# Kernel tuning notes

Measured on AMD Instinct MI355X. Metric: run time of the kernel, lower is better.

## Reference

```python
import jax, jax.numpy as jnp
import numpy as np

T, B, IN_DIM, D_VALUE, D_KEY = 1024, 8, 512, 64, 64
EPS = 1e-8

def setup_inputs() -> dict:
    key = jax.random.key(0)
    ks = jax.random.split(key, 7)
    s = 1.0 / np.sqrt(IN_DIM)
    return {
        "x":  jax.random.normal(ks[0], (T, B, IN_DIM), dtype=jnp.float32),
        "Wv": jax.random.uniform(ks[1], (D_VALUE, IN_DIM), jnp.float32, -s, s),
        "bv": jax.random.uniform(ks[2], (D_VALUE,), jnp.float32, -s, s),
        "Wk": jax.random.uniform(ks[3], (D_KEY, IN_DIM), jnp.float32, -s, s),
        "bk": jax.random.uniform(ks[4], (D_KEY,), jnp.float32, -s, s),
        "Wa": jax.random.uniform(ks[5], (D_KEY, IN_DIM), jnp.float32, -s, s),
        "ba": jax.random.uniform(ks[6], (D_KEY,), jnp.float32, -s, s),
    }

def reference(x, Wv, bv, Wk, bk, Wa, ba):
    # Projections: x (T,B,in_dim) -> v (T,B,d), k (T,B,n), alpha (T,B,n)
    v = jnp.einsum('tbi,di->tbd', x, Wv) + bv
    k = jnp.einsum('tbi,ni->tbn', x, Wk) + bk
    alpha = jax.nn.sigmoid(jnp.einsum('tbi,ni->tbn', x, Wa) + ba)
    # outer product per timestep: (T,B,d,n)
    outer = jnp.einsum('tbd,tbn->tbdn', v, k)
    # log-space cumulative decay, normalized by final cumprod
    log_cumprod = jnp.cumsum(jnp.log(jnp.maximum(alpha, EPS)), axis=0)  # (T,B,n)
    cumprod = jnp.exp(log_cumprod)
    decay = cumprod / (cumprod[-1:] + EPS)
    weighted = outer * decay[:, :, None, :]  # (T,B,d,n)
    S = jnp.cumsum(weighted, axis=0)
    return S
```

## Files before the change

### kernel.cpp

```cpp
#include <hip/hip_runtime.h>
#include <math.h>

#define T_DIM  1024
#define B_DIM  8
#define IN_D   512
#define NROWS  (T_DIM * B_DIM)
#define EPSF   1e-8f
#define LOG_EPS (-18.4206807f)

#define CHUNK  16
#define NCHUNK (T_DIM / CHUNK)
#define SEG    16
#define NSEG   (T_DIM / SEG)

typedef float vfloat4 __attribute__((ext_vector_type(4)));

#define OFF_WT   0
#define OFF_V    (OFF_WT + IN_D * 192)
#define OFF_K    (OFF_V  + NROWS * 64)
#define OFF_Z    (OFF_K  + NROWS * 64)
#define OFF_SEG  (OFF_Z  + NROWS * 64)
#define OFF_TOT  (OFF_SEG + NSEG * B_DIM * 64)
#define OFF_P    (OFF_TOT + B_DIM * 64)
#define OFF_WB   (OFF_P + NCHUNK * B_DIM * 4096)

#define FMA4(A, W, C) \
    (C).x = fmaf((A), (W).x, (C).x); (C).y = fmaf((A), (W).y, (C).y); \
    (C).z = fmaf((A), (W).z, (C).z); (C).w = fmaf((A), (W).w, (C).w);

__global__ void k0_wt(const float* __restrict__ Wv, const float* __restrict__ Wk,
                      const float* __restrict__ Wa, float* __restrict__ Wt,
                      float* __restrict__ seg) {
    int idx = blockIdx.x * 256 + threadIdx.x;
    if (idx < NSEG * 512) seg[idx] = 0.f;
    int i = idx / 192, c = idx % 192;
    float v;
    if (c < 64)       v = Wv[c * IN_D + i];
    else if (c < 128) v = Wk[(c - 64) * IN_D + i];
    else              v = Wa[(c - 128) * IN_D + i];
    Wt[i * 192 + c] = v;
}

__global__ __launch_bounds__(256) void k1_proj(
        const float* __restrict__ x, const float* __restrict__ Wt,
        const float* __restrict__ bv, const float* __restrict__ bk, const float* __restrict__ ba,
        float* __restrict__ V, float* __restrict__ Kb, float* __restrict__ Zb,
        float* __restrict__ seg) {
    __shared__ float smem[14336];
    const int tid = threadIdx.x;
    const int h   = tid >> 6;
    const int sl  = h >> 1;
    const int kk0 = (h & 1) * 16;
    const int t6  = tid & 63;
    const int rq  = t6 >> 4;
    const int cq  = t6 & 15;
    const int row0 = blockIdx.x * 32;

    float4 acc[8][3];
#pragma unroll
    for (int j = 0; j < 8; ++j)
#pragma unroll
        for (int m = 0; m < 3; ++m) acc[j][m] = make_float4(0.f, 0.f, 0.f, 0.f);

    for (int s = 0; s < 8; ++s) {
#pragma unroll
        for (int q = 0; q < 2; ++q) {
            int idx = tid + q * 256;
            int hh = idx >> 8, r = idx & 31, f = (idx >> 5) & 7;
            float4 v4 = reinterpret_cast<const float4*>(x)[((row0 + r) * IN_D + hh * 256 + s * 32 + f * 4) >> 2];
            smem[hh * 1024 + (f * 4 + 0) * 32 + r] = v4.x;
            smem[hh * 1024 + (f * 4 + 1) * 32 + r] = v4.y;
            smem[hh * 1024 + (f * 4 + 2) * 32 + r] = v4.z;
            smem[hh * 1024 + (f * 4 + 3) * 32 + r] = v4.w;
        }
#pragma unroll
        for (int q = 0; q < 12; ++q) {
            int idx = tid + q * 256;
            int hh = idx / 1536;
            int rem = idx - hh * 1536;
            int kk = rem / 48;
            int f  = rem - kk * 48;
            float4 v4 = reinterpret_cast<const float4*>(Wt)[((hh * 256 + s * 32 + kk) * 192 + f * 4) >> 2];
            *reinterpret_cast<float4*>(&smem[2048 + hh * 6144 + kk * 192 + f * 4]) = v4;
        }
        __syncthreads();

#pragma unroll 4
        for (int k16 = 0; k16 < 16; ++k16) {
            const int kk = kk0 + k16;
            const float* xp = &smem[sl * 1024 + kk * 32 + rq * 8];
            float4 xv0 = *reinterpret_cast<const float4*>(xp);
            float4 xv1 = *reinterpret_cast<const float4*>(xp + 4);
            const float* wp = &smem[2048 + sl * 6144 + kk * 192 + cq * 4];
            float4 w0 = *reinterpret_cast<const float4*>(wp);
            float4 w1 = *reinterpret_cast<const float4*>(wp + 64);
            float4 w2 = *reinterpret_cast<const float4*>(wp + 128);
#pragma unroll
            for (int j = 0; j < 4; ++j) {
                float a0 = (&xv0.x)[j];
                float a1 = (&xv1.x)[j];
                FMA4(a0, w0, acc[j][0]); FMA4(a0, w1, acc[j][1]); FMA4(a0, w2, acc[j][2]);
                FMA4(a1, w0, acc[j + 4][0]); FMA4(a1, w1, acc[j + 4][1]); FMA4(a1, w2, acc[j + 4][2]);
            }
        }
        __syncthreads();
    }

    float* red = smem;
    if (h == 1 || h == 3) {
        float* rg = red + (h >> 1) * 6144;
#pragma unroll
        for (int jr = 0; jr < 8; ++jr)
#pragma unroll
            for (int m = 0; m < 3; ++m)
#pragma unroll
                for (int c = 0; c < 4; ++c)
                    rg[((jr * 3 + m) * 4 + c) * 64 + t6] = (&acc[jr][m].x)[c];
    }
    __syncthreads();
    if (h == 0 || h == 2) {
        float* rg = red + (h >> 1) * 6144;
#pragma unroll
        for (int jr = 0; jr < 8; ++jr)
#pragma unroll
            for (int m = 0; m < 3; ++m)
#pragma unroll
                for (int c = 0; c < 4; ++c)
                    (&acc[jr][m].x)[c] += rg[((jr * 3 + m) * 4 + c) * 64 + t6];
    }
    __syncthreads();
    if (h == 2) {
#pragma unroll
        for (int jr = 0; jr < 8; ++jr)
#pragma unroll
            for (int m = 0; m < 3; ++m)
#pragma unroll
                for (int c = 0; c < 4; ++c)
                    red[((jr * 3 + m) * 4 + c) * 64 + t6] = (&acc[jr][m].x)[c];
    }
    __syncthreads();
    if (h == 0) {
#pragma unroll
        for (int jr = 0; jr < 8; ++jr)
#pragma unroll
            for (int m = 0; m < 3; ++m)
#pragma unroll
                for (int c = 0; c < 4; ++c)
                    (&acc[jr][m].x)[c] += red[((jr * 3 + m) * 4 + c) * 64 + t6];

        float4 bv4 = *reinterpret_cast<const float4*>(&bv[cq * 4]);
        float4 bk4 = *reinterpret_cast<const float4*>(&bk[cq * 4]);
        float4 ba4 = *reinterpret_cast<const float4*>(&ba[cq * 4]);
#pragma unroll
        for (int jr = 0; jr < 8; ++jr) {
            int row = row0 + rq * 8 + jr;
            float4 r0, r1, z2, l4;
            r0.x = acc[jr][0].x + bv4.x; r0.y = acc[jr][0].y + bv4.y;
            r0.z = acc[jr][0].z + bv4.z; r0.w = acc[jr][0].w + bv4.w;
            r1.x = acc[jr][1].x + bk4.x; r1.y = acc[jr][1].y + bk4.y;
            r1.z = acc[jr][1].z + bk4.z; r1.w = acc[jr][1].w + bk4.w;
            z2.x = acc[jr][2].x + ba4.x; z2.y = acc[jr][2].y + ba4.y;
            z2.z = acc[jr][2].z + ba4.z; z2.w = acc[jr][2].w + ba4.w;
            l4.x = fmaxf(-log1pf(expf(-z2.x)), LOG_EPS);
            l4.y = fmaxf(-log1pf(expf(-z2.y)), LOG_EPS);
            l4.z = fmaxf(-log1pf(expf(-z2.z)), LOG_EPS);
            l4.w = fmaxf(-log1pf(expf(-z2.w)), LOG_EPS);
            *reinterpret_cast<float4*>(&V [row * 64 + cq * 4]) = r0;
            *reinterpret_cast<float4*>(&Kb[row * 64 + cq * 4]) = r1;
            *reinterpret_cast<float4*>(&Zb[row * 64 + cq * 4]) = l4;
            float* sp = &seg[(row >> 7) * 512 + (row & 7) * 64 + cq * 4];
            atomicAdd(sp + 0, l4.x);
            atomicAdd(sp + 1, l4.y);
            atomicAdd(sp + 2, l4.z);
            atomicAdd(sp + 3, l4.w);
        }
    }
}

__global__ __launch_bounds__(256) void k3_partial(const float* __restrict__ V,
                                                  const float* __restrict__ Z,
                                                  const float* __restrict__ seg,
                                                  const float* __restrict__ Kb,
                                                  float* __restrict__ P,
                                                  float* __restrict__ Wb) {
    __shared__ float vs[CHUNK * 64];
    __shared__ float wsh[CHUNK * 64];
    __shared__ float gsum[4 * 64];
    int b = blockIdx.x & 7, cch = blockIdx.x >> 3;
    int tid = threadIdx.x;
    int dg = tid >> 4, n4 = tid & 15;
    int n = tid & 63, g = tid >> 6;
    int base = b * 64 + n;
    int il = tid >> 4, f = tid & 15;

    float4 v4 = reinterpret_cast<const float4*>(V)[((cch * CHUNK + il) * 8 + b) * 16 + f];

    float run = 0.f, total = 0.f;
#pragma unroll 8
    for (int s2 = 0; s2 < NSEG; ++s2) {
        float sv = seg[s2 * 512 + base];
        if (s2 < cch) run += sv;
        total += sv;
    }
    float invden = 1.f / (expf(total) + EPSF);

    int t0 = cch * CHUNK + g * 4;
    float l0 = Z[(t0 + 0) * 512 + base];
    float l1 = Z[(t0 + 1) * 512 + base];
    float l2 = Z[(t0 + 2) * 512 + base];
    float l3 = Z[(t0 + 3) * 512 + base];
    float k0v = Kb[(t0 + 0) * 512 + base];
    float k1v = Kb[(t0 + 1) * 512 + base];
    float k2v = Kb[(t0 + 2) * 512 + base];
    float k3v = Kb[(t0 + 3) * 512 + base];
    gsum[g * 64 + n] = l0 + l1 + l2 + l3;
    reinterpret_cast<float4*>(vs)[il * 16 + f] = v4;
    __syncthreads();
    float pre = run;
#pragma unroll
    for (int g2 = 0; g2 < 3; ++g2) if (g2 < g) pre += gsum[g2 * 64 + n];
    float c0 = pre + l0, c1 = c0 + l1, c2 = c1 + l2, c3 = c2 + l3;
    wsh[(g * 4 + 0) * 64 + n] = k0v * expf(c0) * invden;
    wsh[(g * 4 + 1) * 64 + n] = k1v * expf(c1) * invden;
    wsh[(g * 4 + 2) * 64 + n] = k2v * expf(c2) * invden;
    wsh[(g * 4 + 3) * 64 + n] = k3v * expf(c3) * invden;
    __syncthreads();

    reinterpret_cast<float4*>(Wb)[(cch * 8 + b) * 256 + il * 16 + f] =
        reinterpret_cast<const float4*>(wsh)[il * 16 + f];

    float4 acc[4];
#pragma unroll
    for (int q = 0; q < 4; ++q) acc[q] = make_float4(0.f, 0.f, 0.f, 0.f);

#pragma unroll
    for (int i = 0; i < CHUNK; ++i) {
        float4 wv = reinterpret_cast<const float4*>(wsh)[i * 16 + n4];
#pragma unroll
        for (int q = 0; q < 4; ++q) {
            float vd = vs[i * 64 + dg + 16 * q];
            acc[q].x = fmaf(vd, wv.x, acc[q].x);
            acc[q].y = fmaf(vd, wv.y, acc[q].y);
            acc[q].z = fmaf(vd, wv.z, acc[q].z);
            acc[q].w = fmaf(vd, wv.w, acc[q].w);
        }
    }
    float* Pp = P + (cch * 8 + b) * 4096;
#pragma unroll
    for (int q = 0; q < 4; ++q)
        *reinterpret_cast<float4*>(Pp + (dg + 16 * q) * 64 + 4 * n4) = acc[q];
}

__global__ __launch_bounds__(256) void k4_prefix(float* __restrict__ P) {
    int gid = blockIdx.x * 256 + threadIdx.x;
    int b = gid >> 12, dn = gid & 4095;
    float run = 0.f;
#pragma unroll
    for (int c = 0; c < NCHUNK; ++c) {
        float v = P[(c * 8 + b) * 4096 + dn];
        P[(c * 8 + b) * 4096 + dn] = run;
        run += v;
    }
}

__global__ __launch_bounds__(256) void k5_main(const float* __restrict__ V,
                                               const float* __restrict__ Wb,
                                               const float* __restrict__ P,
                                               float* __restrict__ S) {
    __shared__ float vs[CHUNK * 64];
    __shared__ float wsh[CHUNK * 64];
    int b = blockIdx.x & 7, cch = blockIdx.x >> 3;
    int tid = threadIdx.x;
    int dg = tid >> 4, n4 = tid & 15;
    int il = tid >> 4, f = tid & 15;

    float4 v4 = reinterpret_cast<const float4*>(V)[((cch * CHUNK + il) * 8 + b) * 16 + f];
    float4 w4 = reinterpret_cast<const float4*>(Wb)[(cch * 8 + b) * 256 + il * 16 + f];
    vfloat4 acc[4];
    const float* Pp = P + (cch * 8 + b) * 4096;
#pragma unroll
    for (int q = 0; q < 4; ++q)
        acc[q] = *reinterpret_cast<const vfloat4*>(Pp + (dg + 16 * q) * 64 + 4 * n4);
    reinterpret_cast<float4*>(vs)[il * 16 + f]  = v4;
    reinterpret_cast<float4*>(wsh)[il * 16 + f] = w4;
    __syncthreads();

#pragma unroll
    for (int i = 0; i < CHUNK; ++i) {
        float4 wv = reinterpret_cast<const float4*>(wsh)[i * 16 + n4];
        int t = cch * CHUNK + i;
        float* Sb = S + (size_t)t * 32768 + b * 4096;
#pragma unroll
        for (int q = 0; q < 4; ++q) {
            float vd = vs[i * 64 + dg + 16 * q];
            acc[q].x = fmaf(vd, wv.x, acc[q].x);
            acc[q].y = fmaf(vd, wv.y, acc[q].y);
            acc[q].z = fmaf(vd, wv.z, acc[q].z);
            acc[q].w = fmaf(vd, wv.w, acc[q].w);
            __builtin_nontemporal_store(acc[q],
                reinterpret_cast<vfloat4*>(Sb + (dg + 16 * q) * 64 + 4 * n4));
        }
    }
}

extern "C" void kernel_launch(void* const* d_in, const int* in_sizes, int n_in,
                              void* d_out, int out_size, void* d_ws, size_t ws_size,
                              hipStream_t stream) {
    const float* x  = (const float*)d_in[0];
    const float* Wv = (const float*)d_in[1];
    const float* bv = (const float*)d_in[2];
    const float* Wk = (const float*)d_in[3];
    const float* bk = (const float*)d_in[4];
    const float* Wa = (const float*)d_in[5];
    const float* ba = (const float*)d_in[6];
    float* S  = (float*)d_out;
    float* ws = (float*)d_ws;

    float* Wt  = ws + OFF_WT;
    float* V   = ws + OFF_V;
    float* Kb  = ws + OFF_K;
    float* Zb  = ws + OFF_Z;
    float* seg = ws + OFF_SEG;
    float* P   = ws + OFF_P;
    float* Wb  = ws + OFF_WB;

    k0_wt     <<<384, 256, 0, stream>>>(Wv, Wk, Wa, Wt, seg);
    k1_proj   <<<256, 256, 0, stream>>>(x, Wt, bv, bk, ba, V, Kb, Zb, seg);
    k3_partial<<<512, 256, 0, stream>>>(V, Zb, seg, Kb, P, Wb);
    k4_prefix <<<128, 256, 0, stream>>>(P);
    k5_main   <<<512, 256, 0, stream>>>(V, Wb, P, S);
}
```

Baseline: 219.6 us.

## Fuse projection, partial, prefix and main kernels into one persistent kernel with grid barriers

```diff
diff --git a/kernel.cpp b/kernel.cpp
--- a/kernel.cpp
+++ b/kernel.cpp
@@ -12,6 +12,8 @@
 #define NCHUNK (T_DIM / CHUNK)
 #define SEG    16
 #define NSEG   (T_DIM / SEG)
+
+#define NBLK   512u
 
 typedef float vfloat4 __attribute__((ext_vector_type(4)));
 
@@ -23,16 +25,31 @@
 #define OFF_TOT  (OFF_SEG + NSEG * B_DIM * 64)
 #define OFF_P    (OFF_TOT + B_DIM * 64)
 #define OFF_WB   (OFF_P + NCHUNK * B_DIM * 4096)
+#define OFF_BAR  (OFF_WB + 524288)
 
 #define FMA4(A, W, C) \
     (C).x = fmaf((A), (W).x, (C).x); (C).y = fmaf((A), (W).y, (C).y); \
     (C).z = fmaf((A), (W).z, (C).z); (C).w = fmaf((A), (W).w, (C).w);
 
-__global__ void k0_wt(const float* __restrict__ Wv, const float* __restrict__ Wk,
-                      const float* __restrict__ Wa, float* __restrict__ Wt,
-                      float* __restrict__ seg) {
+__device__ __forceinline__ void gridbar(unsigned* bar, int slot) {
+    __threadfence();
+    __syncthreads();
+    if (threadIdx.x == 0) {
+        atomicAdd(&bar[slot], 1u);
+        while (__hip_atomic_load(&bar[slot], __ATOMIC_RELAXED,
+                                 __HIP_MEMORY_SCOPE_AGENT) < NBLK)
+            __builtin_amdgcn_s_sleep(2);
+        __threadfence();
+    }
+    __syncthreads();
+}
+
+__global__ void kpre(const float* __restrict__ Wv, const float* __restrict__ Wk,
+                     const float* __restrict__ Wa, float* __restrict__ Wt,
+                     float* __restrict__ seg, unsigned* __restrict__ bar) {
     int idx = blockIdx.x * 256 + threadIdx.x;
     if (idx < NSEG * 512) seg[idx] = 0.f;
+    if (idx < 16) bar[idx] = 0u;
     int i = idx / 192, c = idx % 192;
     float v;
     if (c < 64)       v = Wv[c * IN_D + i];
@@ -41,264 +58,266 @@
     Wt[i * 192 + c] = v;
 }
 
-__global__ __launch_bounds__(256) void k1_proj(
+__global__ __launch_bounds__(256, 2) void kfused(
         const float* __restrict__ x, const float* __restrict__ Wt,
         const float* __restrict__ bv, const float* __restrict__ bk, const float* __restrict__ ba,
         float* __restrict__ V, float* __restrict__ Kb, float* __restrict__ Zb,
-        float* __restrict__ seg) {
+        float* __restrict__ seg, float* __restrict__ P, float* __restrict__ Wb,
+        float* __restrict__ S, unsigned* __restrict__ bar) {
     __shared__ float smem[14336];
+    const int blk = blockIdx.x;
     const int tid = threadIdx.x;
-    const int h   = tid >> 6;
-    const int sl  = h >> 1;
-    const int kk0 = (h & 1) * 16;
-    const int t6  = tid & 63;
-    const int rq  = t6 >> 4;
-    const int cq  = t6 & 15;
-    const int row0 = blockIdx.x * 32;
-
-    float4 acc[8][3];
-#pragma unroll
-    for (int j = 0; j < 8; ++j)
-#pragma unroll
-        for (int m = 0; m < 3; ++m) acc[j][m] = make_float4(0.f, 0.f, 0.f, 0.f);
-
-    for (int s = 0; s < 8; ++s) {
-#pragma unroll
-        for (int q = 0; q < 2; ++q) {
-            int idx = tid + q * 256;
-            int hh = idx >> 8, r = idx & 31, f = (idx >> 5) & 7;
-            float4 v4 = reinterpret_cast<const float4*>(x)[((row0 + r) * IN_D + hh * 256 + s * 32 + f * 4) >> 2];
-            smem[hh * 1024 + (f * 4 + 0) * 32 + r] = v4.x;
-            smem[hh * 1024 + (f * 4 + 1) * 32 + r] = v4.y;
-            smem[hh * 1024 + (f * 4 + 2) * 32 + r] = v4.z;
-            smem[hh * 1024 + (f * 4 + 3) * 32 + r] = v4.w;
-        }
-#pragma unroll
-        for (int q = 0; q < 12; ++q) {
-            int idx = tid + q * 256;
-            int hh = idx / 1536;
-            int rem = idx - hh * 1536;
-            int kk = rem / 48;
-            int f  = rem - kk * 48;
-            float4 v4 = reinterpret_cast<const float4*>(Wt)[((hh * 256 + s * 32 + kk) * 192 + f * 4) >> 2];
-            *reinterpret_cast<float4*>(&smem[2048 + hh * 6144 + kk * 192 + f * 4]) = v4;
-        }
-        __syncthreads();
+
+    if (blk < 256) {
+        const int h   = tid >> 6;
+        const int sl  = h >> 1;
+        const int kk0 = (h & 1) * 16;
+        const int t6  = tid & 63;
+        const int rq  = t6 >> 4;
+        const int cq  = t6 & 15;
+        const int row0 = blk * 32;
+
+        float4 acc[8][3];
+#pragma unroll
+        for (int j = 0; j < 8; ++j)
+#pragma unroll
+            for (int m = 0; m < 3; ++m) acc[j][m] = make_float4(0.f, 0.f, 0.f, 0.f);
+
+        for (int s = 0; s < 8; ++s) {
+#pragma unroll
+            for (int q = 0; q < 2; ++q) {
+                int idx = tid + q * 256;
+                int hh = idx >> 8, r = idx & 31, f = (idx >> 5) & 7;
+                float4 v4 = reinterpret_cast<const float4*>(x)[((row0 + r) * IN_D + hh * 256 + s * 32 + f * 4) >> 2];
+                smem[hh * 1024 + (f * 4 + 0) * 32 + r] = v4.x;
+                smem[hh * 1024 + (f * 4 + 1) * 32 + r] = v4.y;
+                smem[hh * 1024 + (f * 4 + 2) * 32 + r] = v4.z;
+                smem[hh * 1024 + (f * 4 + 3) * 32 + r] = v4.w;
+            }
+#pragma unroll
+            for (int q = 0; q < 12; ++q) {
+                int idx = tid + q * 256;
+                int hh = idx / 1536;
+                int rem = idx - hh * 1536;
+                int kk = rem / 48;
+                int f  = rem - kk * 48;
+                float4 v4 = reinterpret_cast<const float4*>(Wt)[((hh * 256 + s * 32 + kk) * 192 + f * 4) >> 2];
+                *reinterpret_cast<float4*>(&smem[2048 + hh * 6144 + kk * 192 + f * 4]) = v4;
+            }
+            __syncthreads();
 
 #pragma unroll 4
-        for (int k16 = 0; k16 < 16; ++k16) {
-            const int kk = kk0 + k16;
-            const float* xp = &smem[sl * 1024 + kk * 32 + rq * 8];
-            float4 xv0 = *reinterpret_cast<const float4*>(xp);
-            float4 xv1 = *reinterpret_cast<const float4*>(xp + 4);
-            const float* wp = &smem[2048 + sl * 6144 + kk * 192 + cq * 4];
-            float4 w0 = *reinterpret_cast<const float4*>(wp);
-            float4 w1 = *reinterpret_cast<const float4*>(wp + 64);
-            float4 w2 = *reinterpret_cast<const float4*>(wp + 128);
-#pragma unroll
-            for (int j = 0; j < 4; ++j) {
-                float a0 = (&xv0.x)[j];
-                float a1 = (&xv1.x)[j];
-                FMA4(a0, w0, acc[j][0]); FMA4(a0, w1, acc[j][1]); FMA4(a0, w2, acc[j][2]);
-                FMA4(a1, w0, acc[j + 4][0]); FMA4(a1, w1, acc[j + 4][1]); FMA4(a1, w2, acc[j + 4][2]);
-            }
-        }
-        __syncthreads();
-    }
-
-    float* red = smem;
-    if (h == 1 || h == 3) {
-        float* rg = red + (h >> 1) * 6144;
-#pragma unroll
-        for (int jr = 0; jr < 8; ++jr)
-#pragma unroll
-            for (int m = 0; m < 3; ++m)
-#pragma unroll
-                for (int c = 0; c < 4; ++c)
-                    rg[((jr * 3 + m) * 4 + c) * 64 + t6] = (&acc[jr][m].x)[c];
-    }
-    __syncthreads();
-    if (h == 0 || h == 2) {
-        float* rg = red + (h >> 1) * 6144;
-#pragma unroll
-        for (int jr = 0; jr < 8; ++jr)
-#pragma unroll
-            for (int m = 0; m < 3; ++m)
-#pragma unroll
-                for (int c = 0; c < 4; ++c)
-                    (&acc[jr][m].x)[c] += rg[((jr * 3 + m) * 4 + c) * 64 + t6];
-    }
-    __syncthreads();
-    if (h == 2) {
-#pragma unroll
-        for (int jr = 0; jr < 8; ++jr)
-#pragma unroll
-            for (int m = 0; m < 3; ++m)
-#pragma unroll
-                for (int c = 0; c < 4; ++c)
-                    red[((jr * 3 + m) * 4 + c) * 64 + t6] = (&acc[jr][m].x)[c];
-    }
-    __syncthreads();
-    if (h == 0) {
-#pragma unroll
-        for (int jr = 0; jr < 8; ++jr)
-#pragma unroll
-            for (int m = 0; m < 3; ++m)
-#pragma unroll
-                for (int c = 0; c < 4; ++c)
-                    (&acc[jr][m].x)[c] += red[((jr * 3 + m) * 4 + c) * 64 + t6];
-
-        float4 bv4 = *reinterpret_cast<const float4*>(&bv[cq * 4]);
-        float4 bk4 = *reinterpret_cast<const float4*>(&bk[cq * 4]);
-        float4 ba4 = *reinterpret_cast<const float4*>(&ba[cq * 4]);
-#pragma unroll
-        for (int jr = 0; jr < 8; ++jr) {
-            int row = row0 + rq * 8 + jr;
-            float4 r0, r1, z2, l4;
-            r0.x = acc[jr][0].x + bv4.x; r0.y = acc[jr][0].y + bv4.y;
-            r0.z = acc[jr][0].z + bv4.z; r0.w = acc[jr][0].w + bv4.w;
-            r1.x = acc[jr][1].x + bk4.x; r1.y = acc[jr][1].y + bk4.y;
-            r1.z = acc[jr][1].z + bk4.z; r1.w = acc[jr][1].w + bk4.w;
-            z2.x = acc[jr][2].x + ba4.x; z2.y = acc[jr][2].y + ba4.y;
-            z2.z = acc[jr][2].z + ba4.z; z2.w = acc[jr][2].w + ba4.w;
-            l4.x = fmaxf(-log1pf(expf(-z2.x)), LOG_EPS);
-            l4.y = fmaxf(-log1pf(expf(-z2.y)), LOG_EPS);
-            l4.z = fmaxf(-log1pf(expf(-z2.z)), LOG_EPS);
-            l4.w = fmaxf(-log1pf(expf(-z2.w)), LOG_EPS);
-            *reinterpret_cast<float4*>(&V [row * 64 + cq * 4]) = r0;
-            *reinterpret_cast<float4*>(&Kb[row * 64 + cq * 4]) = r1;
-            *reinterpret_cast<float4*>(&Zb[row * 64 + cq * 4]) = l4;
-            float* sp = &seg[(row >> 7) * 512 + (row & 7) * 64 + cq * 4];
-            atomicAdd(sp + 0, l4.x);
-            atomicAdd(sp + 1, l4.y);
-            atomicAdd(sp + 2, l4.z);
-            atomicAdd(sp + 3, l4.w);
-        }
-    }
-}
-
-__global__ __launch_bounds__(256) void k3_partial(const float* __restrict__ V,
-                                                  const float* __restrict__ Z,
-                                                  const float* __restrict__ seg,
-                                                  const float* __restrict__ Kb,
-                                                  float* __restrict__ P,
-                                                  float* __restrict__ Wb) {
-    __shared__ float vs[CHUNK * 64];
-    __shared__ float wsh[CHUNK * 64];
-    __shared__ float gsum[4 * 64];
-    int b = blockIdx.x & 7, cch = blockIdx.x >> 3;
-    int tid = threadIdx.x;
-    int dg = tid >> 4, n4 = tid & 15;
-    int n = tid & 63, g = tid >> 6;
-    int base = b * 64 + n;
-    int il = tid >> 4, f = tid & 15;
-
-    float4 v4 = reinterpret_cast<const float4*>(V)[((cch * CHUNK + il) * 8 + b) * 16 + f];
-
-    float run = 0.f, total = 0.f;
+            for (int k16 = 0; k16 < 16; ++k16) {
+                const int kk = kk0 + k16;
+                const float* xp = &smem[sl * 1024 + kk * 32 + rq * 8];
+                float4 xv0 = *reinterpret_cast<const float4*>(xp);
+                float4 xv1 = *reinterpret_cast<const float4*>(xp + 4);
+                const float* wp = &smem[2048 + sl * 6144 + kk * 192 + cq * 4];
+                float4 w0 = *reinterpret_cast<const float4*>(wp);
+                float4 w1 = *reinterpret_cast<const float4*>(wp + 64);
+                float4 w2 = *reinterpret_cast<const float4*>(wp + 128);
+#pragma unroll
+                for (int j = 0; j < 4; ++j) {
+                    float a0 = (&xv0.x)[j];
+                    float a1 = (&xv1.x)[j];
+                    FMA4(a0, w0, acc[j][0]); FMA4(a0, w1, acc[j][1]); FMA4(a0, w2, acc[j][2]);
+                    FMA4(a1, w0, acc[j + 4][0]); FMA4(a1, w1, acc[j + 4][1]); FMA4(a1, w2, acc[j + 4][2]);
+                }
+            }
+            __syncthreads();
+        }
+
+        float* red = smem;
+        if (h == 1 || h == 3) {
+            float* rg = red + (h >> 1) * 6144;
+#pragma unroll
+            for (int jr = 0; jr < 8; ++jr)
+#pragma unroll
+                for (int m = 0; m < 3; ++m)
+#pragma unroll
+                    for (int c = 0; c < 4; ++c)
+                        rg[((jr * 3 + m) * 4 + c) * 64 + t6] = (&acc[jr][m].x)[c];
+        }
+        __syncthreads();
+        if (h == 0 || h == 2) {
+            float* rg = red + (h >> 1) * 6144;
+#pragma unroll
+            for (int jr = 0; jr < 8; ++jr)
+#pragma unroll
+                for (int m = 0; m < 3; ++m)
+#pragma unroll
+                    for (int c = 0; c < 4; ++c)
+                        (&acc[jr][m].x)[c] += rg[((jr * 3 + m) * 4 + c) * 64 + t6];
+        }
+        __syncthreads();
+        if (h == 2) {
+#pragma unroll
+            for (int jr = 0; jr < 8; ++jr)
+#pragma unroll
+                for (int m = 0; m < 3; ++m)
+#pragma unroll
+                    for (int c = 0; c < 4; ++c)
+                        red[((jr * 3 + m) * 4 + c) * 64 + t6] = (&acc[jr][m].x)[c];
+        }
+        __syncthreads();
+        if (h == 0) {
+#pragma unroll
+            for (int jr = 0; jr < 8; ++jr)
+#pragma unroll
+                for (int m = 0; m < 3; ++m)
+#pragma unroll
+                    for (int c = 0; c < 4; ++c)
+                        (&acc[jr][m].x)[c] += red[((jr * 3 + m) * 4 + c) * 64 + t6];
+
+            float4 bv4 = *reinterpret_cast<const float4*>(&bv[cq * 4]);
+            float4 bk4 = *reinterpret_cast<const float4*>(&bk[cq * 4]);
+            float4 ba4 = *reinterpret_cast<const float4*>(&ba[cq * 4]);
+#pragma unroll
+            for (int jr = 0; jr < 8; ++jr) {
+                int row = row0 + rq * 8 + jr;
+                float4 r0, r1, z2, l4;
+                r0.x = acc[jr][0].x + bv4.x; r0.y = acc[jr][0].y + bv4.y;
+                r0.z = acc[jr][0].z + bv4.z; r0.w = acc[jr][0].w + bv4.w;
+                r1.x = acc[jr][1].x + bk4.x; r1.y = acc[jr][1].y + bk4.y;
+                r1.z = acc[jr][1].z + bk4.z; r1.w = acc[jr][1].w + bk4.w;
+                z2.x = acc[jr][2].x + ba4.x; z2.y = acc[jr][2].y + ba4.y;
+                z2.z = acc[jr][2].z + ba4.z; z2.w = acc[jr][2].w + ba4.w;
+                l4.x = fmaxf(-log1pf(expf(-z2.x)), LOG_EPS);
+                l4.y = fmaxf(-log1pf(expf(-z2.y)), LOG_EPS);
+                l4.z = fmaxf(-log1pf(expf(-z2.z)), LOG_EPS);
+                l4.w = fmaxf(-log1pf(expf(-z2.w)), LOG_EPS);
+                *reinterpret_cast<float4*>(&V [row * 64 + cq * 4]) = r0;
+                *reinterpret_cast<float4*>(&Kb[row * 64 + cq * 4]) = r1;
+                *reinterpret_cast<float4*>(&Zb[row * 64 + cq * 4]) = l4;
+                float* sp = &seg[(row >> 7) * 512 + (row & 7) * 64 + cq * 4];
+                atomicAdd(sp + 0, l4.x);
+                atomicAdd(sp + 1, l4.y);
+                atomicAdd(sp + 2, l4.z);
+                atomicAdd(sp + 3, l4.w);
+            }
+        }
+    }
+
+    gridbar(bar, 0);
+
+    {
+        float* vs   = smem;
+        float* wsh  = smem + 1024;
+        float* gsum = smem + 2048;
+        int b = blk & 7, cch = blk >> 3;
+        int dg = tid >> 4, n4 = tid & 15;
+        int n = tid & 63, g = tid >> 6;
+        int base = b * 64 + n;
+        int il = tid >> 4, f = tid & 15;
+
+        float4 v4 = reinterpret_cast<const float4*>(V)[((cch * CHUNK + il) * 8 + b) * 16 + f];
+
+        float run = 0.f, total = 0.f;
 #pragma unroll 8
-    for (int s2 = 0; s2 < NSEG; ++s2) {
-        float sv = seg[s2 * 512 + base];
-        if (s2 < cch) run += sv;
-        total += sv;
-    }
-    float invden = 1.f / (expf(total) + EPSF);
-
-    int t0 = cch * CHUNK + g * 4;
-    float l0 = Z[(t0 + 0) * 512 + base];
-    float l1 = Z[(t0 + 1) * 512 + base];
-    float l2 = Z[(t0 + 2) * 512 + base];
-    float l3 = Z[(t0 + 3) * 512 + base];
-    float k0v = Kb[(t0 + 0) * 512 + base];
-    float k1v = Kb[(t0 + 1) * 512 + base];
-    float k2v = Kb[(t0 + 2) * 512 + base];
-    float k3v = Kb[(t0 + 3) * 512 + base];
-    gsum[g * 64 + n] = l0 + l1 + l2 + l3;
-    reinterpret_cast<float4*>(vs)[il * 16 + f] = v4;
-    __syncthreads();
-    float pre = run;
-#pragma unroll
-    for (int g2 = 0; g2 < 3; ++g2) if (g2 < g) pre += gsum[g2 * 64 + n];
-    float c0 = pre + l0, c1 = c0 + l1, c2 = c1 + l2, c3 = c2 + l3;
-    wsh[(g * 4 + 0) * 64 + n] = k0v * expf(c0) * invden;
-    wsh[(g * 4 + 1) * 64 + n] = k1v * expf(c1) * invden;
-    wsh[(g * 4 + 2) * 64 + n] = k2v * expf(c2) * invden;
-    wsh[(g * 4 + 3) * 64 + n] = k3v * expf(c3) * invden;
-    __syncthreads();
-
-    reinterpret_cast<float4*>(Wb)[(cch * 8 + b) * 256 + il * 16 + f] =
-        reinterpret_cast<const float4*>(wsh)[il * 16 + f];
-
-    float4 acc[4];
-#pragma unroll
-    for (int q = 0; q < 4; ++q) acc[q] = make_float4(0.f, 0.f, 0.f, 0.f);
-
-#pragma unroll
-    for (int i = 0; i < CHUNK; ++i) {
-        float4 wv = reinterpret_cast<const float4*>(wsh)[i * 16 + n4];
-#pragma unroll
-        for (int q = 0; q < 4; ++q) {
-            float vd = vs[i * 64 + dg + 16 * q];
-            acc[q].x = fmaf(vd, wv.x, acc[q].x);
-            acc[q].y = fmaf(vd, wv.y, acc[q].y);
-            acc[q].z = fmaf(vd, wv.z, acc[q].z);
-            acc[q].w = fmaf(vd, wv.w, acc[q].w);
-        }
-    }
-    float* Pp = P + (cch * 8 + b) * 4096;
-#pragma unroll
-    for (int q = 0; q < 4; ++q)
-        *reinterpret_cast<float4*>(Pp + (dg + 16 * q) * 64 + 4 * n4) = acc[q];
-}
-
-__global__ __launch_bounds__(256) void k4_prefix(float* __restrict__ P) {
-    int gid = blockIdx.x * 256 + threadIdx.x;
-    int b = gid >> 12, dn = gid & 4095;
-    float run = 0.f;
-#pragma unroll
-    for (int c = 0; c < NCHUNK; ++c) {
-        float v = P[(c * 8 + b) * 4096 + dn];
-        P[(c * 8 + b) * 4096 + dn] = run;
-        run += v;
-    }
-}
-
-__global__ __launch_bounds__(256) void k5_main(const float* __restrict__ V,
-                                               const float* __restrict__ Wb,
-                                               const float* __restrict__ P,
-                                               float* __restrict__ S) {
-    __shared__ float vs[CHUNK * 64];
-    __shared__ float wsh[CHUNK * 64];
-    int b = blockIdx.x & 7, cch = blockIdx.x >> 3;
-    int tid = threadIdx.x;
-    int dg = tid >> 4, n4 = tid & 15;
-    int il = tid >> 4, f = tid & 15;
-
-    float4 v4 = reinterpret_cast<const float4*>(V)[((cch * CHUNK + il) * 8 + b) * 16 + f];
-    float4 w4 = reinterpret_cast<const float4*>(Wb)[(cch * 8 + b) * 256 + il * 16 + f];
-    vfloat4 acc[4];
-    const float* Pp = P + (cch * 8 + b) * 4096;
-#pragma unroll
-    for (int q = 0; q < 4; ++q)
-        acc[q] = *reinterpret_cast<const vfloat4*>(Pp + (dg + 16 * q) * 64 + 4 * n4);
-    reinterpret_cast<float4*>(vs)[il * 16 + f]  = v4;
-    reinterpret_cast<float4*>(wsh)[il * 16 + f] = w4;
-    __syncthreads();
-
-#pragma unroll
-    for (int i = 0; i < CHUNK; ++i) {
-        float4 wv = reinterpret_cast<const float4*>(wsh)[i * 16 + n4];
-        int t = cch * CHUNK + i;
-        float* Sb = S + (size_t)t * 32768 + b * 4096;
-#pragma unroll
-        for (int q = 0; q < 4; ++q) {
-            float vd = vs[i * 64 + dg + 16 * q];
-            acc[q].x = fmaf(vd, wv.x, acc[q].x);
-            acc[q].y = fmaf(vd, wv.y, acc[q].y);
-            acc[q].z = fmaf(vd, wv.z, acc[q].z);
-            acc[q].w = fmaf(vd, wv.w, acc[q].w);
-            __builtin_nontemporal_store(acc[q],
-                reinterpret_cast<vfloat4*>(Sb + (dg + 16 * q) * 64 + 4 * n4));
+        for (int s2 = 0; s2 < NSEG; ++s2) {
+            float sv = seg[s2 * 512 + base];
+            if (s2 < cch) run += sv;
+            total += sv;
+        }
+        float invden = 1.f / (expf(total) + EPSF);
+
+        int t0 = cch * CHUNK + g * 4;
+        float l0 = Zb[(t0 + 0) * 512 + base];
+        float l1 = Zb[(t0 + 1) * 512 + base];
+        float l2 = Zb[(t0 + 2) * 512 + base];
+        float l3 = Zb[(t0 + 3) * 512 + base];
+        float k0v = Kb[(t0 + 0) * 512 + base];
+        float k1v = Kb[(t0 + 1) * 512 + base];
+        float k2v = Kb[(t0 + 2) * 512 + base];
+        float k3v = Kb[(t0 + 3) * 512 + base];
+        gsum[g * 64 + n] = l0 + l1 + l2 + l3;
+        reinterpret_cast<float4*>(vs)[il * 16 + f] = v4;
+        __syncthreads();
+        float pre = run;
+#pragma unroll
+        for (int g2 = 0; g2 < 3; ++g2) if (g2 < g) pre += gsum[g2 * 64 + n];
+        float c0 = pre + l0, c1 = c0 + l1, c2 = c1 + l2, c3 = c2 + l3;
+        wsh[(g * 4 + 0) * 64 + n] = k0v * expf(c0) * invden;
+        wsh[(g * 4 + 1) * 64 + n] = k1v * expf(c1) * invden;
+        wsh[(g * 4 + 2) * 64 + n] = k2v * expf(c2) * invden;
+        wsh[(g * 4 + 3) * 64 + n] = k3v * expf(c3) * invden;
+        __syncthreads();
+
+        reinterpret_cast<float4*>(Wb)[(cch * 8 + b) * 256 + il * 16 + f] =
+            reinterpret_cast<const float4*>(wsh)[il * 16 + f];
+
+        float4 acc[4];
+#pragma unroll
+        for (int q = 0; q < 4; ++q) acc[q] = make_float4(0.f, 0.f, 0.f, 0.f);
+
+#pragma unroll
+        for (int i = 0; i < CHUNK; ++i) {
+            float4 wv = reinterpret_cast<const float4*>(wsh)[i * 16 + n4];
+#pragma unroll
+            for (int q = 0; q < 4; ++q) {
+                float vd = vs[i * 64 + dg + 16 * q];
+                acc[q].x = fmaf(vd, wv.x, acc[q].x);
+                acc[q].y = fmaf(vd, wv.y, acc[q].y);
+                acc[q].z = fmaf(vd, wv.z, acc[q].z);
+                acc[q].w = fmaf(vd, wv.w, acc[q].w);
+            }
+        }
+        float* Pp = P + (cch * 8 + b) * 4096;
+#pragma unroll
+        for (int q = 0; q < 4; ++q)
+            *reinterpret_cast<float4*>(Pp + (dg + 16 * q) * 64 + 4 * n4) = acc[q];
+    }
+
+    gridbar(bar, 1);
+
+    if (blk < 128) {
+        int gid = blk * 256 + tid;
+        int b = gid >> 12, dn = gid & 4095;
+        float run = 0.f;
+#pragma unroll
+        for (int c = 0; c < NCHUNK; ++c) {
+            float v = P[(c * 8 + b) * 4096 + dn];
+            P[(c * 8 + b) * 4096 + dn] = run;
+            run += v;
+        }
+    }
+
+    gridbar(bar, 2);
+
+    {
+        float* vs  = smem;
+        float* wsh = smem + 1024;
+        int b = blk & 7, cch = blk >> 3;
+        int dg = tid >> 4, n4 = tid & 15;
+        int il = tid >> 4, f = tid & 15;
+
+        __syncthreads();
+        float4 v4 = reinterpret_cast<const float4*>(V)[((cch * CHUNK + il) * 8 + b) * 16 + f];
+        float4 w4 = reinterpret_cast<const float4*>(Wb)[(cch * 8 + b) * 256 + il * 16 + f];
+        vfloat4 acc[4];
+        const float* Pp = P + (cch * 8 + b) * 4096;
+#pragma unroll
+        for (int q = 0; q < 4; ++q)
+            acc[q] = *reinterpret_cast<const vfloat4*>(Pp + (dg + 16 * q) * 64 + 4 * n4);
+        reinterpret_cast<float4*>(vs)[il * 16 + f]  = v4;
+        reinterpret_cast<float4*>(wsh)[il * 16 + f] = w4;
+        __syncthreads();
+
+#pragma unroll
+        for (int i = 0; i < CHUNK; ++i) {
+            float4 wv = reinterpret_cast<const float4*>(wsh)[i * 16 + n4];
+            int t = cch * CHUNK + i;
+            float* Sb = S + (size_t)t * 32768 + b * 4096;
+#pragma unroll
+            for (int q = 0; q < 4; ++q) {
+                float vd = vs[i * 64 + dg + 16 * q];
+                acc[q].x = fmaf(vd, wv.x, acc[q].x);
+                acc[q].y = fmaf(vd, wv.y, acc[q].y);
+                acc[q].z = fmaf(vd, wv.z, acc[q].z);
+                acc[q].w = fmaf(vd, wv.w, acc[q].w);
+                __builtin_nontemporal_store(acc[q],
+                    reinterpret_cast<vfloat4*>(Sb + (dg + 16 * q) * 64 + 4 * n4));
+            }
         }
     }
 }
@@ -323,10 +342,8 @@
     float* seg = ws + OFF_SEG;
     float* P   = ws + OFF_P;
     float* Wb  = ws + OFF_WB;
-
-    k0_wt     <<<384, 256, 0, stream>>>(Wv, Wk, Wa, Wt, seg);
-    k1_proj   <<<256, 256, 0, stream>>>(x, Wt, bv, bk, ba, V, Kb, Zb, seg);
-    k3_partial<<<512, 256, 0, stream>>>(V, Zb, seg, Kb, P, Wb);
-    k4_prefix <<<128, 256, 0, stream>>>(P);
-    k5_main   <<<512, 256, 0, stream>>>(V, Wb, P, S);
+    unsigned* bar = (unsigned*)(ws + OFF_BAR);
+
+    kpre  <<<384, 256, 0, stream>>>(Wv, Wk, Wa, Wt, seg, bar);
+    kfused<<<NBLK, 256, 0, stream>>>(x, Wt, bv, bk, ba, V, Kb, Zb, seg, P, Wb, S, bar);
 }
```

Measured after the change: 431.0 us. +96.3%, slower.
